# Kernel tuning notes

Hardware: AMD Instinct MI355X
Metric: run time of the kernel (lower is better)

The kernel has to match this reference:

```python
import jax, jax.numpy as jnp
import numpy as np

B, S, D, H = 4, 1024, 1024, 16
DH = D // H  # 64
SCALE = 1.0 / np.sqrt(DH)


def setup_inputs() -> dict:
    key = jax.random.key(0)
    ks = jax.random.split(key, 12)
    std = 0.02
    inp = {
        "query": jax.random.normal(ks[0], (B, S, D), jnp.float32),
        "key": jax.random.normal(ks[1], (B, S, D), jnp.float32),
        "value": jax.random.normal(ks[2], (B, S, D), jnp.float32),
        # all-ones mask: exercises masked_fill path without the NaN the
        # head-axis softmax would produce for any masked entry
        "mask": jnp.ones((1, S, S), jnp.int32),
        "Wq": jax.random.normal(ks[3], (D, D), jnp.float32) * std,
        "bq": jnp.zeros((D,), jnp.float32),
        "Wk": jax.random.normal(ks[4], (D, D), jnp.float32) * std,
        "bk": jnp.zeros((D,), jnp.float32),
        "Wv": jax.random.normal(ks[5], (D, D), jnp.float32) * std,
        "bv": jnp.zeros((D,), jnp.float32),
        "Wo": jax.random.normal(ks[6], (D, D), jnp.float32) * std,
        "bo": jnp.zeros((D,), jnp.float32),
    }
    return inp


def reference(query, key, value, mask, Wq, bq, Wk, bk, Wv, bv, Wo, bo):
    # project and split heads: [B, S, D] -> [B, S, H, DH]
    q = (query @ Wq + bq).reshape(B, S, H, DH)
    k = (key @ Wk + bk).reshape(B, S, H, DH)
    v = (value @ Wv + bv).reshape(B, S, H, DH)

    # scores [B, i, j, H]
    scores = jnp.einsum("bihd,bjhd->bijh", q, k) * SCALE
    # mask [1, i, j] broadcast over heads via trailing axis (unsqueeze(-1))
    scores = jnp.where(mask[..., None] == 0, -jnp.inf, scores)
    # faithful to source: nn.Softmax(dim=-1) on bijh layout -> softmax over HEADS
    attn = jax.nn.softmax(scores, axis=-1)
    # dropout in eval mode (identity)
    x = jnp.einsum("bijh,bjhd->bihd", attn, v).reshape(B, S, D)
    return x @ Wo + bo
```

## Files before the change

### kernel.cpp

```cpp
#include <hip/hip_runtime.h>
#include <hip/hip_bf16.h>


using f32x4  = __attribute__((ext_vector_type(4))) float;
using f32x2  = __attribute__((ext_vector_type(2))) float;
using bf16x8 = __attribute__((ext_vector_type(8))) short;
using bf16x4 = __attribute__((ext_vector_type(4))) short;

__device__ inline unsigned short f2b(float f){
    unsigned u = __float_as_uint(f);
    unsigned r = (u + 0x7fffu + ((u >> 16) & 1u)) >> 16;
    return (unsigned short)r;
}
__device__ inline float b2f(unsigned short s){
    return __uint_as_float(((unsigned)s) << 16);
}

#define GLL16(gp, lp) __builtin_amdgcn_global_load_lds( \
    (const __attribute__((address_space(1))) void*)(gp), \
    (__attribute__((address_space(3))) void*)(lp), 16, 0, 0)

#define LGKM0 do { asm volatile("s_waitcnt lgkmcnt(0)" ::: "memory"); \
                   __builtin_amdgcn_sched_barrier(0); } while(0)
#define BAR   do { __builtin_amdgcn_s_barrier(); \
                   __builtin_amdgcn_sched_barrier(0); } while(0)

__global__ __launch_bounds__(256) void convert_qkv(
    const float* __restrict__ q, const float* __restrict__ k, const float* __restrict__ v,
    unsigned short* __restrict__ dst)
{
    const long gid = (long)blockIdx.x * 256 + threadIdx.x;
    const int  t   = (int)(gid >> 20);
    const long off = (gid & 1048575) << 2;
    const float* src = (t == 0) ? q : (t == 1) ? k : v;
    const float4 x = *(const float4*)(src + off);
    ushort4 o;
    o.x = f2b(x.x); o.y = f2b(x.y); o.z = f2b(x.z); o.w = f2b(x.w);
    *(ushort4*)(dst + (long)t * 4194304 + off) = o;
}

__global__ __launch_bounds__(256) void wtrans(
    const float* __restrict__ w0, const float* __restrict__ w1,
    const float* __restrict__ w2, const float* __restrict__ w3,
    unsigned short* __restrict__ out)
{
    const float* W = (blockIdx.z == 0) ? w0 : (blockIdx.z == 1) ? w1 : (blockIdx.z == 2) ? w2 : w3;
    unsigned short* O = out + (long)blockIdx.z * 1048576;
    __shared__ float t[32][33];
    const int n0 = blockIdx.x * 32, k0 = blockIdx.y * 32;
    const int tx = threadIdx.x, ty = threadIdx.y;
    #pragma unroll
    for (int i = 0; i < 4; i++)
        t[ty + 8*i][tx] = W[(long)(k0 + ty + 8*i) * 1024 + n0 + tx];
    __syncthreads();
    #pragma unroll
    for (int i = 0; i < 4; i++)
        O[(long)(n0 + ty + 8*i) * 1024 + k0 + tx] = f2b(t[tx][ty + 8*i]);
}

__global__ __launch_bounds__(256) void vtrans(
    const unsigned short* __restrict__ V, unsigned short* __restrict__ Vt)
{
    const int b = blockIdx.z;
    __shared__ unsigned short t[32][33];
    const int s0 = blockIdx.x * 32, d0 = blockIdx.y * 32;
    const int tx = threadIdx.x, ty = threadIdx.y;
    #pragma unroll
    for (int i = 0; i < 4; i++)
        t[ty + 8*i][tx] = V[(long)(b*1024 + s0 + ty + 8*i) * 1024 + d0 + tx];
    __syncthreads();
    #pragma unroll
    for (int i = 0; i < 4; i++)
        Vt[(long)b * 1048576 + (long)(d0 + ty + 8*i) * 1024 + s0 + tx] = t[tx][ty + 8*i];
}

template<int OUTF32>
__device__ __forceinline__ void gemm_body(
    const unsigned short* __restrict__ A,
    const unsigned short* __restrict__ BT,
    const float* __restrict__ bias,
    void* __restrict__ Cout, int N, int K,
    unsigned short* As, unsigned short* Bs)
{
    const int tid  = threadIdx.x;
    const int wave = tid >> 6, lane = tid & 63;
    const int l15  = lane & 15, l4 = lane >> 4;
    const int wr   = wave >> 1, wc = wave & 1;
    const long rowBase = (long)blockIdx.x * 128;
    const long colBase = (long)blockIdx.y * 128;

    f32x4 acc[4][4];
    #pragma unroll
    for (int m = 0; m < 4; m++)
        #pragma unroll
        for (int n = 0; n < 4; n++)
            acc[m][n] = (f32x4){0.f, 0.f, 0.f, 0.f};

    const int c0    = wave * 2;
    const int srow0 = c0 * 16 + (lane >> 2);
    const int srow1 = srow0 + 16;
    const int skk   = (lane & 3) * 8;

    for (int k0 = 0; k0 < K; k0 += 32) {
        GLL16(A  + (rowBase + srow0) * K + k0 + skk, As + c0 * 512);
        GLL16(A  + (rowBase + srow1) * K + k0 + skk, As + (c0 + 1) * 512);
        GLL16(BT + (colBase + srow0) * K + k0 + skk, Bs + c0 * 512);
        GLL16(BT + (colBase + srow1) * K + k0 + skk, Bs + (c0 + 1) * 512);
        __syncthreads();
        bf16x8 af[4], bfr[4];
        #pragma unroll
        for (int m = 0; m < 4; m++)
            af[m] = *(const bf16x8*)(As + (wr*64 + m*16 + l15) * 32 + l4 * 8);
        #pragma unroll
        for (int n = 0; n < 4; n++)
            bfr[n] = *(const bf16x8*)(Bs + (wc*64 + n*16 + l15) * 32 + l4 * 8);
        #pragma unroll
        for (int m = 0; m < 4; m++)
            #pragma unroll
            for (int n = 0; n < 4; n++)
                acc[m][n] = __builtin_amdgcn_mfma_f32_16x16x32_bf16(af[m], bfr[n], acc[m][n], 0, 0, 0);
        __syncthreads();
    }

    #pragma unroll
    for (int m = 0; m < 4; m++) {
        const long row = rowBase + wr*64 + m*16 + l4*4;
        #pragma unroll
        for (int n = 0; n < 4; n++) {
            const long col = colBase + wc*64 + n*16 + l15;
            const float bv = bias[col];
            #pragma unroll
            for (int r = 0; r < 4; r++) {
                const float vv = acc[m][n][r] + bv;
                if (OUTF32) ((float*)Cout)[(row + r) * N + col] = vv;
                else        ((unsigned short*)Cout)[(row + r) * N + col] = f2b(vv);
            }
        }
    }
}

__global__ __launch_bounds__(256) void gemm_bias_f32(
    const unsigned short* __restrict__ A,
    const unsigned short* __restrict__ BT,
    const float* __restrict__ bias,
    float* __restrict__ Cout, int N, int K)
{
    __shared__ unsigned short As[128 * 32];
    __shared__ unsigned short Bs[128 * 32];
    gemm_body<1>(A, BT, bias, (void*)Cout, N, K, As, Bs);
}

__global__ __launch_bounds__(256) void gemm3(
    const unsigned short* __restrict__ Abase,
    const unsigned short* __restrict__ WT,
    const float* __restrict__ bq, const float* __restrict__ bk, const float* __restrict__ bv,
    unsigned short* __restrict__ Cbase)
{
    __shared__ unsigned short As[128 * 32];
    __shared__ unsigned short Bs[128 * 32];
    const int z = blockIdx.z;
    const unsigned short* A  = Abase + (long)z * 4194304;
    const unsigned short* BT = WT    + (long)z * 1048576;
    unsigned short*       C  = Cbase + (long)z * 4194304;
    const float* bias = (z == 0) ? bq : (z == 1) ? bk : bv;
    gemm_body<0>(A, BT, bias, (void*)C, 1024, 1024, As, Bs);
}

__global__ __launch_bounds__(512, 2) void attn_fused(
    const unsigned short* __restrict__ Q,
    const unsigned short* __restrict__ Kg_,
    const unsigned short* __restrict__ Vt,
    const int* __restrict__ mask,
    unsigned short* __restrict__ P0,
    unsigned short* __restrict__ P1)
{
    __shared__ __align__(16) unsigned char smem[73728];
    float*         Se = (float*)smem;
    float*         So = (float*)(smem + 36864);
    unsigned char* Pb = smem;

    const int tid = threadIdx.x, w = tid >> 6, lane = tid & 63;
    const int l15 = lane & 15, l4 = lane >> 4;
    const int h0  = 2 * w;
    const int sxor = h0 ^ (l4 << 2);

    const int bid = blockIdx.x;
    const int wg  = (bid & 7) * 32 + (bid >> 3);
    const int b   = wg >> 6;
    const int jh  = (wg >> 5) & 1;
    const int i0  = (wg & 31) << 5;
    const int jbase = jh << 9;

    const unsigned short* Kb = Kg_ + (long)b * 1048576;
    const unsigned short* Vb = Vt  + (long)b * 1048576;
    unsigned short* Pout = (jh == 0) ? P0 : P1;

    const int si = tid >> 4, sj = tid & 15;
    const int xorv = si & 12;
    const int mrow = (i0 + si) * 1024 + jbase;

    bf16x8 qf[2][2][2];
    #pragma unroll
    for (int is = 0; is < 2; is++)
        #pragma unroll
        for (int hh = 0; hh < 2; hh++)
            #pragma unroll
            for (int ks = 0; ks < 2; ks++)
                qf[is][hh][ks] = *(const bf16x8*)(Q + (long)(b*1024 + i0 + is*16 + l15) * 1024
                                                  + (h0 + hh) * 64 + ks * 32 + l4 * 8);

#define LOAD_KF(J0) do { \
    _Pragma("unroll") \
    for (int t_ = 0; t_ < 2; t_++) \
        _Pragma("unroll") \
        for (int hh = 0; hh < 2; hh++) \
            _Pragma("unroll") \
            for (int ks = 0; ks < 2; ks++) \
                kf[t_][hh][ks] = *(const bf16x8*)(Kb + (long)((J0) + t_*16 + l15) * 1024 \
                                                   + (h0 + hh) * 64 + ks * 32 + l4 * 8); \
    } while(0)

#define LOAD_VF(J0) do { \
    _Pragma("unroll") \
    for (int hh = 0; hh < 2; hh++) \
        _Pragma("unroll") \
        for (int n = 0; n < 4; n++) \
            vf[hh][n] = *(const bf16x8*)(Vb + (long)((h0 + hh) * 64 + n * 16 + l15) * 1024 \
                                           + (J0) + l4 * 8); \
    } while(0)

    bf16x8 kf[2][2][2];
    bf16x8 vf[2][4];
    LOAD_KF(jbase);
    LOAD_VF(jbase);

    f32x4 acc[2][2][4];
    #pragma unroll
    for (int is = 0; is < 2; is++)
        #pragma unroll
        for (int hh = 0; hh < 2; hh++)
            #pragma unroll
            for (int n = 0; n < 4; n++)
                acc[is][hh][n] = (f32x4){0.f, 0.f, 0.f, 0.f};

    for (int g = 0; g < 16; ++g) {
        const int j0 = jbase + g * 32;
        const int mke = mask[mrow + g * 32 + sj];
        const int mko = mask[mrow + g * 32 + 16 + sj];

        #pragma unroll
        for (int t_ = 0; t_ < 2; t_++) {
            float* St = t_ ? So : Se;
            #pragma unroll
            for (int is = 0; is < 2; is++) {
                f32x4 sv0 = (f32x4){0.f,0.f,0.f,0.f}, sv1 = (f32x4){0.f,0.f,0.f,0.f};
                sv0 = __builtin_amdgcn_mfma_f32_16x16x32_bf16(qf[is][0][0], kf[t_][0][0], sv0, 0, 0, 0);
                sv0 = __builtin_amdgcn_mfma_f32_16x16x32_bf16(qf[is][0][1], kf[t_][0][1], sv0, 0, 0, 0);
                sv1 = __builtin_amdgcn_mfma_f32_16x16x32_bf16(qf[is][1][0], kf[t_][1][0], sv1, 0, 0, 0);
                sv1 = __builtin_amdgcn_mfma_f32_16x16x32_bf16(qf[is][1][1], kf[t_][1][1], sv1, 0, 0, 0);
                #pragma unroll
                for (int r = 0; r < 4; r++) {
                    const int ij = (is*16 + l4*4 + r) * 16 + l15;
                    f32x2 pr; pr[0] = sv0[r]; pr[1] = sv1[r];
                    *(f32x2*)(St + ij * 18 + sxor) = pr;
                }
            }
        }
        LGKM0; BAR;

        if (g < 15) LOAD_KF(j0 + 32);

        unsigned pe[8];
        {
            const float* sp = Se + tid * 18;
            float tv[16];
            #pragma unroll
            for (int q_ = 0; q_ < 8; q_++) {
                const f32x2 t2 = *(const f32x2*)(sp + q_ * 2);
                tv[q_*2] = t2[0]; tv[q_*2+1] = t2[1];
            }
            float Z = 0.f;
            #pragma unroll
            for (int h = 0; h < 16; h++) {
                float x = tv[h] * 0.18033688f;
                if (mke == 0) x = -__builtin_inff();
                float e; asm("v_exp_f32 %0, %1" : "=v"(e) : "v"(x));
                tv[h] = e; Z += e;
            }
            float inv; asm("v_rcp_f32 %0, %1" : "=v"(inv) : "v"(Z));
            #pragma unroll
            for (int h = 0; h < 8; h++) {
                const unsigned lo = (__float_as_uint(tv[2*h]   * inv) + 0x8000u) >> 16;
                const unsigned hi = (__float_as_uint(tv[2*h+1] * inv) + 0x8000u) >> 16;
                pe[h] = lo | (hi << 16);
            }
        }
        BAR;
        #pragma unroll
        for (int h = 0; h < 16; h++) {
            const unsigned short pv = (unsigned short)((h & 1) ? (pe[h >> 1] >> 16) : pe[h >> 1]);
            *(unsigned short*)(Pb + (h ^ xorv) * 2304 + si * 72 + sj * 2) = pv;
        }

        {
            const float* sp = So + tid * 18;
            float tv[16];
            #pragma unroll
            for (int q_ = 0; q_ < 8; q_++) {
                const f32x2 t2 = *(const f32x2*)(sp + q_ * 2);
                tv[q_*2] = t2[0]; tv[q_*2+1] = t2[1];
            }
            float Z = 0.f;
            #pragma unroll
            for (int h = 0; h < 16; h++) {
                float x = tv[h] * 0.18033688f;
                if (mko == 0) x = -__builtin_inff();
                float e; asm("v_exp_f32 %0, %1" : "=v"(e) : "v"(x));
                tv[h] = e; Z += e;
            }
            float inv; asm("v_rcp_f32 %0, %1" : "=v"(inv) : "v"(Z));
            #pragma unroll
            for (int h = 0; h < 16; h++) {
                const unsigned p16 = (__float_as_uint(tv[h] * inv) + 0x8000u) >> 16;
                *(unsigned short*)(Pb + (h ^ xorv) * 2304 + si * 72 + 32 + sj * 2) = (unsigned short)p16;
            }
        }
        LGKM0; BAR;

        {
            bf16x8 pa[2][2];
            #pragma unroll
            for (int is = 0; is < 2; is++)
                #pragma unroll
                for (int hh = 0; hh < 2; hh++) {
                    const unsigned char* pr = Pb + (h0 + hh) * 2304 + (is*16 + l15) * 72 + l4 * 16;
                    bf16x4 lo = *(const bf16x4*)(pr);
                    bf16x4 hi = *(const bf16x4*)(pr + 8);
                    pa[is][hh] = (bf16x8){lo[0],lo[1],lo[2],lo[3], hi[0],hi[1],hi[2],hi[3]};
                }
            #pragma unroll
            for (int is = 0; is < 2; is++)
                #pragma unroll
                for (int hh = 0; hh < 2; hh++)
                    #pragma unroll
                    for (int n = 0; n < 4; n++)
                        acc[is][hh][n] = __builtin_amdgcn_mfma_f32_16x16x32_bf16(pa[is][hh], vf[hh][n], acc[is][hh][n], 0, 0, 0);
        }
        if (g < 15) {
            LOAD_VF(j0 + 32);
            BAR;
        }
    }

    #pragma unroll
    for (int is = 0; is < 2; is++)
        #pragma unroll
        for (int hh = 0; hh < 2; hh++)
            #pragma unroll
            for (int n = 0; n < 4; n++)
                #pragma unroll
                for (int r = 0; r < 4; r++) {
                    const long row = b * 1024 + i0 + is * 16 + l4 * 4 + r;
                    Pout[row * 1024 + (h0 + hh) * 64 + n * 16 + l15] = f2b(acc[is][hh][n][r]);
                }
#undef LOAD_KF
#undef LOAD_VF
}

__global__ __launch_bounds__(256) void addp(
    unsigned short* __restrict__ P0, const unsigned short* __restrict__ P1)
{
    const long i = ((long)blockIdx.x * 256 + threadIdx.x) * 8;
    ushort4 a0 = *(const ushort4*)(P0 + i);
    ushort4 a1 = *(const ushort4*)(P0 + i + 4);
    ushort4 b0 = *(const ushort4*)(P1 + i);
    ushort4 b1 = *(const ushort4*)(P1 + i + 4);
    ushort4 o0, o1;
    o0.x = f2b(b2f(a0.x) + b2f(b0.x)); o0.y = f2b(b2f(a0.y) + b2f(b0.y));
    o0.z = f2b(b2f(a0.z) + b2f(b0.z)); o0.w = f2b(b2f(a0.w) + b2f(b0.w));
    o1.x = f2b(b2f(a1.x) + b2f(b1.x)); o1.y = f2b(b2f(a1.y) + b2f(b1.y));
    o1.z = f2b(b2f(a1.z) + b2f(b1.z)); o1.w = f2b(b2f(a1.w) + b2f(b1.w));
    *(ushort4*)(P0 + i) = o0;
    *(ushort4*)(P0 + i + 4) = o1;
}

extern "C" void kernel_launch(void* const* d_in, const int* in_sizes, int n_in,
                              void* d_out, int out_size, void* d_ws, size_t ws_size,
                              hipStream_t stream)
{
    const float* q    = (const float*)d_in[0];
    const float* k    = (const float*)d_in[1];
    const float* v    = (const float*)d_in[2];
    const int*   mask = (const int*)  d_in[3];
    const float* Wq   = (const float*)d_in[4];
    const float* bq   = (const float*)d_in[5];
    const float* Wk   = (const float*)d_in[6];
    const float* bk   = (const float*)d_in[7];
    const float* Wv   = (const float*)d_in[8];
    const float* bv   = (const float*)d_in[9];
    const float* Wo   = (const float*)d_in[10];
    const float* bo   = (const float*)d_in[11];

    unsigned short* ws = (unsigned short*)d_ws;
    const long MS = 1048576;
    unsigned short* WT  = ws;
    unsigned short* Xq  = ws + 4*MS;
    unsigned short* Xk  = ws + 8*MS;
    unsigned short* Xv  = ws + 12*MS;
    unsigned short* Qm  = ws + 16*MS;
    unsigned short* Km  = ws + 20*MS;
    unsigned short* Vm  = ws + 24*MS;
    unsigned short* Vtm = Xq;
    unsigned short* P0  = Xk;
    unsigned short* P1  = Vm;

    convert_qkv<<<12288, 256, 0, stream>>>(q, k, v, Xq);
    wtrans<<<dim3(32, 32, 4), dim3(32, 8), 0, stream>>>(Wq, Wk, Wv, Wo, WT);
    gemm3<<<dim3(32, 8, 3), 256, 0, stream>>>(Xq, WT, bq, bk, bv, Qm);
    vtrans<<<dim3(32, 32, 4), dim3(32, 8), 0, stream>>>(Vm, Vtm);
    attn_fused<<<256, 512, 0, stream>>>(Qm, Km, Vtm, mask, P0, P1);
    addp<<<2048, 256, 0, stream>>>(P0, P1);
    gemm_bias_f32<<<dim3(32, 8), 256, 0, stream>>>(P0, WT + 3*MS, bo, (float*)d_out, 1024, 1024);
}
```

Measured before the change: 170.4 us.

## Halve attention query tile to 16 rows and double grid to 512 blocks

```diff
diff --git a/kernel.cpp b/kernel.cpp
--- a/kernel.cpp
+++ b/kernel.cpp
@@ -174,9 +174,8 @@
     unsigned short* __restrict__ P0,
     unsigned short* __restrict__ P1)
 {
-    __shared__ __align__(16) unsigned char smem[73728];
-    float*         Se = (float*)smem;
-    float*         So = (float*)(smem + 36864);
+    __shared__ __align__(16) unsigned char smem[36864];
+    float*         S  = (float*)smem;
     unsigned char* Pb = smem;
 
     const int tid = threadIdx.x, w = tid >> 6, lane = tid & 63;
@@ -185,29 +184,27 @@
     const int sxor = h0 ^ (l4 << 2);
 
     const int bid = blockIdx.x;
-    const int wg  = (bid & 7) * 32 + (bid >> 3);
-    const int b   = wg >> 6;
-    const int jh  = (wg >> 5) & 1;
-    const int i0  = (wg & 31) << 5;
+    const int wg  = (bid & 7) * 64 + (bid >> 3);
+    const int b   = wg >> 7;
+    const int jh  = (wg >> 6) & 1;
+    const int i0  = (wg & 63) << 4;
     const int jbase = jh << 9;
 
     const unsigned short* Kb = Kg_ + (long)b * 1048576;
     const unsigned short* Vb = Vt  + (long)b * 1048576;
     unsigned short* Pout = (jh == 0) ? P0 : P1;
 
-    const int si = tid >> 4, sj = tid & 15;
-    const int xorv = si & 12;
-    const int mrow = (i0 + si) * 1024 + jbase;
-
-    bf16x8 qf[2][2][2];
-    #pragma unroll
-    for (int is = 0; is < 2; is++)
-        #pragma unroll
-        for (int hh = 0; hh < 2; hh++)
-            #pragma unroll
-            for (int ks = 0; ks < 2; ks++)
-                qf[is][hh][ks] = *(const bf16x8*)(Q + (long)(b*1024 + i0 + is*16 + l15) * 1024
-                                                  + (h0 + hh) * 64 + ks * 32 + l4 * 8);
+    const int i_sm = tid >> 5, j_sm = tid & 31;
+    const int xorv = i_sm & 12;
+    const int mrow = (i0 + i_sm) * 1024 + jbase;
+
+    bf16x8 qf[2][2];
+    #pragma unroll
+    for (int hh = 0; hh < 2; hh++)
+        #pragma unroll
+        for (int ks = 0; ks < 2; ks++)
+            qf[hh][ks] = *(const bf16x8*)(Q + (long)(b*1024 + i0 + l15) * 1024
+                                          + (h0 + hh) * 64 + ks * 32 + l4 * 8);
 
 #define LOAD_KF(J0) do { \
     _Pragma("unroll") \
@@ -234,36 +231,29 @@
     LOAD_KF(jbase);
     LOAD_VF(jbase);
 
-    f32x4 acc[2][2][4];
-    #pragma unroll
-    for (int is = 0; is < 2; is++)
-        #pragma unroll
-        for (int hh = 0; hh < 2; hh++)
-            #pragma unroll
-            for (int n = 0; n < 4; n++)
-                acc[is][hh][n] = (f32x4){0.f, 0.f, 0.f, 0.f};
+    f32x4 acc[2][4];
+    #pragma unroll
+    for (int hh = 0; hh < 2; hh++)
+        #pragma unroll
+        for (int n = 0; n < 4; n++)
+            acc[hh][n] = (f32x4){0.f, 0.f, 0.f, 0.f};
 
     for (int g = 0; g < 16; ++g) {
         const int j0 = jbase + g * 32;
-        const int mke = mask[mrow + g * 32 + sj];
-        const int mko = mask[mrow + g * 32 + 16 + sj];
+        const int mk = mask[mrow + g * 32 + j_sm];
 
         #pragma unroll
         for (int t_ = 0; t_ < 2; t_++) {
-            float* St = t_ ? So : Se;
-            #pragma unroll
-            for (int is = 0; is < 2; is++) {
-                f32x4 sv0 = (f32x4){0.f,0.f,0.f,0.f}, sv1 = (f32x4){0.f,0.f,0.f,0.f};
-                sv0 = __builtin_amdgcn_mfma_f32_16x16x32_bf16(qf[is][0][0], kf[t_][0][0], sv0, 0, 0, 0);
-                sv0 = __builtin_amdgcn_mfma_f32_16x16x32_bf16(qf[is][0][1], kf[t_][0][1], sv0, 0, 0, 0);
-                sv1 = __builtin_amdgcn_mfma_f32_16x16x32_bf16(qf[is][1][0], kf[t_][1][0], sv1, 0, 0, 0);
-                sv1 = __builtin_amdgcn_mfma_f32_16x16x32_bf16(qf[is][1][1], kf[t_][1][1], sv1, 0, 0, 0);
-                #pragma unroll
-                for (int r = 0; r < 4; r++) {
-                    const int ij = (is*16 + l4*4 + r) * 16 + l15;
-                    f32x2 pr; pr[0] = sv0[r]; pr[1] = sv1[r];
-                    *(f32x2*)(St + ij * 18 + sxor) = pr;
-                }
+            f32x4 sv0 = (f32x4){0.f,0.f,0.f,0.f}, sv1 = (f32x4){0.f,0.f,0.f,0.f};
+            sv0 = __builtin_amdgcn_mfma_f32_16x16x32_bf16(qf[0][0], kf[t_][0][0], sv0, 0, 0, 0);
+            sv0 = __builtin_amdgcn_mfma_f32_16x16x32_bf16(qf[0][1], kf[t_][0][1], sv0, 0, 0, 0);
+            sv1 = __builtin_amdgcn_mfma_f32_16x16x32_bf16(qf[1][0], kf[t_][1][0], sv1, 0, 0, 0);
+            sv1 = __builtin_amdgcn_mfma_f32_16x16x32_bf16(qf[1][1], kf[t_][1][1], sv1, 0, 0, 0);
+            #pragma unroll
+            for (int r = 0; r < 4; r++) {
+                const int ij = (l4*4 + r) * 32 + t_ * 16 + l15;
+                f32x2 pr; pr[0] = sv0[r]; pr[1] = sv1[r];
+                *(f32x2*)(S + ij * 18 + sxor) = pr;
             }
         }
         LGKM0; BAR;
@@ -272,7 +262,7 @@
 
         unsigned pe[8];
         {
-            const float* sp = Se + tid * 18;
+            const float* sp = S + tid * 18;
             float tv[16];
             #pragma unroll
             for (int q_ = 0; q_ < 8; q_++) {
@@ -283,7 +273,7 @@
             #pragma unroll
             for (int h = 0; h < 16; h++) {
                 float x = tv[h] * 0.18033688f;
-                if (mke == 0) x = -__builtin_inff();
+                if (mk == 0) x = -__builtin_inff();
                 float e; asm("v_exp_f32 %0, %1" : "=v"(e) : "v"(x));
                 tv[h] = e; Z += e;
             }
@@ -299,52 +289,24 @@
         #pragma unroll
         for (int h = 0; h < 16; h++) {
             const unsigned short pv = (unsigned short)((h & 1) ? (pe[h >> 1] >> 16) : pe[h >> 1]);
-            *(unsigned short*)(Pb + (h ^ xorv) * 2304 + si * 72 + sj * 2) = pv;
-        }
+            *(unsigned short*)(Pb + (h ^ xorv) * 1152 + i_sm * 72 + j_sm * 2) = pv;
+        }
+        LGKM0; BAR;
 
         {
-            const float* sp = So + tid * 18;
-            float tv[16];
-            #pragma unroll
-            for (int q_ = 0; q_ < 8; q_++) {
-                const f32x2 t2 = *(const f32x2*)(sp + q_ * 2);
-                tv[q_*2] = t2[0]; tv[q_*2+1] = t2[1];
-            }
-            float Z = 0.f;
-            #pragma unroll
-            for (int h = 0; h < 16; h++) {
-                float x = tv[h] * 0.18033688f;
-                if (mko == 0) x = -__builtin_inff();
-                float e; asm("v_exp_f32 %0, %1" : "=v"(e) : "v"(x));
-                tv[h] = e; Z += e;
-            }
-            float inv; asm("v_rcp_f32 %0, %1" : "=v"(inv) : "v"(Z));
-            #pragma unroll
-            for (int h = 0; h < 16; h++) {
-                const unsigned p16 = (__float_as_uint(tv[h] * inv) + 0x8000u) >> 16;
-                *(unsigned short*)(Pb + (h ^ xorv) * 2304 + si * 72 + 32 + sj * 2) = (unsigned short)p16;
-            }
-        }
-        LGKM0; BAR;
-
-        {
-            bf16x8 pa[2][2];
-            #pragma unroll
-            for (int is = 0; is < 2; is++)
+            bf16x8 pa[2];
+            #pragma unroll
+            for (int hh = 0; hh < 2; hh++) {
+                const unsigned char* pr = Pb + (h0 + hh) * 1152 + l15 * 72 + l4 * 16;
+                bf16x4 lo = *(const bf16x4*)(pr);
+                bf16x4 hi = *(const bf16x4*)(pr + 8);
+                pa[hh] = (bf16x8){lo[0],lo[1],lo[2],lo[3], hi[0],hi[1],hi[2],hi[3]};
+            }
+            #pragma unroll
+            for (int hh = 0; hh < 2; hh++)
                 #pragma unroll
-                for (int hh = 0; hh < 2; hh++) {
-                    const unsigned char* pr = Pb + (h0 + hh) * 2304 + (is*16 + l15) * 72 + l4 * 16;
-                    bf16x4 lo = *(const bf16x4*)(pr);
-                    bf16x4 hi = *(const bf16x4*)(pr + 8);
-                    pa[is][hh] = (bf16x8){lo[0],lo[1],lo[2],lo[3], hi[0],hi[1],hi[2],hi[3]};
-                }
-            #pragma unroll
-            for (int is = 0; is < 2; is++)
-                #pragma unroll
-                for (int hh = 0; hh < 2; hh++)
-                    #pragma unroll
-                    for (int n = 0; n < 4; n++)
-                        acc[is][hh][n] = __builtin_amdgcn_mfma_f32_16x16x32_bf16(pa[is][hh], vf[hh][n], acc[is][hh][n], 0, 0, 0);
+                for (int n = 0; n < 4; n++)
+                    acc[hh][n] = __builtin_amdgcn_mfma_f32_16x16x32_bf16(pa[hh], vf[hh][n], acc[hh][n], 0, 0, 0);
         }
         if (g < 15) {
             LOAD_VF(j0 + 32);
@@ -353,16 +315,14 @@
     }
 
     #pragma unroll
-    for (int is = 0; is < 2; is++)
-        #pragma unroll
-        for (int hh = 0; hh < 2; hh++)
-            #pragma unroll
-            for (int n = 0; n < 4; n++)
-                #pragma unroll
-                for (int r = 0; r < 4; r++) {
-                    const long row = b * 1024 + i0 + is * 16 + l4 * 4 + r;
-                    Pout[row * 1024 + (h0 + hh) * 64 + n * 16 + l15] = f2b(acc[is][hh][n][r]);
-                }
+    for (int hh = 0; hh < 2; hh++)
+        #pragma unroll
+        for (int n = 0; n < 4; n++)
+            #pragma unroll
+            for (int r = 0; r < 4; r++) {
+                const long row = b * 1024 + i0 + l4 * 4 + r;
+                Pout[row * 1024 + (h0 + hh) * 64 + n * 16 + l15] = f2b(acc[hh][n][r]);
+            }
 #undef LOAD_KF
 #undef LOAD_VF
 }
@@ -418,7 +378,7 @@
     wtrans<<<dim3(32, 32, 4), dim3(32, 8), 0, stream>>>(Wq, Wk, Wv, Wo, WT);
     gemm3<<<dim3(32, 8, 3), 256, 0, stream>>>(Xq, WT, bq, bk, bv, Qm);
     vtrans<<<dim3(32, 32, 4), dim3(32, 8), 0, stream>>>(Vm, Vtm);
-    attn_fused<<<256, 512, 0, stream>>>(Qm, Km, Vtm, mask, P0, P1);
+    attn_fused<<<512, 512, 0, stream>>>(Qm, Km, Vtm, mask, P0, P1);
     addp<<<2048, 256, 0, stream>>>(P0, P1);
     gemm_bias_f32<<<dim3(32, 8), 256, 0, stream>>>(P0, WT + 3*MS, bo, (float*)d_out, 1024, 1024);
 }
```

Measured after the change: 223.4 us (median of 2 runs). +31.1%, slower.

## Pre-pack K and V into MFMA fragment order for coalesced attention loads

Applied to the files above, without the earlier changes.

```diff
diff --git a/kernel.cpp b/kernel.cpp
--- a/kernel.cpp
+++ b/kernel.cpp
@@ -58,20 +58,54 @@
         O[(long)(n0 + ty + 8*i) * 1024 + k0 + tx] = f2b(t[tx][ty + 8*i]);
 }
 
-__global__ __launch_bounds__(256) void vtrans(
-    const unsigned short* __restrict__ V, unsigned short* __restrict__ Vt)
-{
-    const int b = blockIdx.z;
-    __shared__ unsigned short t[32][33];
-    const int s0 = blockIdx.x * 32, d0 = blockIdx.y * 32;
-    const int tx = threadIdx.x, ty = threadIdx.y;
-    #pragma unroll
-    for (int i = 0; i < 4; i++)
-        t[ty + 8*i][tx] = V[(long)(b*1024 + s0 + ty + 8*i) * 1024 + d0 + tx];
+__global__ __launch_bounds__(256) void kf_trans(
+    const unsigned short* __restrict__ Km, unsigned short* __restrict__ Kf)
+{
+    const int b = blockIdx.y, jt = blockIdx.x;
+    __shared__ unsigned short t[16][1032];
+    const int tid = threadIdx.x;
+    #pragma unroll
+    for (int p = 0; p < 8; p++) {
+        const int idx = p * 2048 + tid * 8;
+        const int r = idx >> 10, c = idx & 1023;
+        *(uint4*)&t[r][c] = *(const uint4*)(Km + (long)(b*1024 + jt*16 + r) * 1024 + c);
+    }
     __syncthreads();
     #pragma unroll
-    for (int i = 0; i < 4; i++)
-        Vt[(long)b * 1048576 + (long)(d0 + ty + 8*i) * 1024 + s0 + tx] = t[tx][ty + 8*i];
+    for (int p = 0; p < 8; p++) {
+        const int o  = p * 2048 + tid * 8;
+        const int hk = o >> 9;
+        const int l  = (o >> 3) & 63;
+        const int cc = (hk >> 1) * 64 + (hk & 1) * 32 + (l >> 4) * 8;
+        *(uint4*)(Kf + (long)(b*64 + jt) * 16384 + o) = *(const uint4*)&t[l & 15][cc];
+    }
+}
+
+__global__ __launch_bounds__(256) void vf_trans(
+    const unsigned short* __restrict__ Vm, unsigned short* __restrict__ Vf)
+{
+    const int b = blockIdx.y, jg = blockIdx.x;
+    __shared__ unsigned short t[32][1032];
+    const int tid = threadIdx.x;
+    #pragma unroll
+    for (int p = 0; p < 16; p++) {
+        const int idx = p * 2048 + tid * 8;
+        const int r = idx >> 10, c = idx & 1023;
+        *(uint4*)&t[r][c] = *(const uint4*)(Vm + (long)(b*1024 + jg*32 + r) * 1024 + c);
+    }
+    __syncthreads();
+    #pragma unroll
+    for (int p = 0; p < 16; p++) {
+        const int o  = p * 2048 + tid * 8;
+        const int hn = o >> 9;
+        const int l  = (o >> 3) & 63;
+        const int col = (hn >> 2) * 64 + (hn & 3) * 16 + (l & 15);
+        const int r0  = (l >> 4) * 8;
+        unsigned short vv[8];
+        #pragma unroll
+        for (int e = 0; e < 8; e++) vv[e] = t[r0 + e][col];
+        *(uint4*)(Vf + (long)(b*32 + jg) * 32768 + o) = *(const uint4*)vv;
+    }
 }
 
 template<int OUTF32>
@@ -168,8 +202,8 @@
 
 __global__ __launch_bounds__(512, 2) void attn_fused(
     const unsigned short* __restrict__ Q,
-    const unsigned short* __restrict__ Kg_,
-    const unsigned short* __restrict__ Vt,
+    const unsigned short* __restrict__ Kf_,
+    const unsigned short* __restrict__ Vf_,
     const int* __restrict__ mask,
     unsigned short* __restrict__ P0,
     unsigned short* __restrict__ P1)
@@ -191,8 +225,8 @@
     const int i0  = (wg & 31) << 5;
     const int jbase = jh << 9;
 
-    const unsigned short* Kb = Kg_ + (long)b * 1048576;
-    const unsigned short* Vb = Vt  + (long)b * 1048576;
+    const unsigned short* Kfb = Kf_ + (long)b * 1048576;
+    const unsigned short* Vfb = Vf_ + (long)b * 1048576;
     unsigned short* Pout = (jh == 0) ? P0 : P1;
 
     const int si = tid >> 4, sj = tid & 15;
@@ -209,30 +243,30 @@
                 qf[is][hh][ks] = *(const bf16x8*)(Q + (long)(b*1024 + i0 + is*16 + l15) * 1024
                                                   + (h0 + hh) * 64 + ks * 32 + l4 * 8);
 
-#define LOAD_KF(J0) do { \
+#define LOAD_KF(JT) do { \
     _Pragma("unroll") \
     for (int t_ = 0; t_ < 2; t_++) \
         _Pragma("unroll") \
         for (int hh = 0; hh < 2; hh++) \
             _Pragma("unroll") \
             for (int ks = 0; ks < 2; ks++) \
-                kf[t_][hh][ks] = *(const bf16x8*)(Kb + (long)((J0) + t_*16 + l15) * 1024 \
-                                                   + (h0 + hh) * 64 + ks * 32 + l4 * 8); \
+                kf[t_][hh][ks] = *(const bf16x8*)(Kfb + ((JT) + t_) * 16384 \
+                                                   + ((h0 + hh) * 2 + ks) * 512 + lane * 8); \
     } while(0)
 
-#define LOAD_VF(J0) do { \
+#define LOAD_VF(JG) do { \
     _Pragma("unroll") \
     for (int hh = 0; hh < 2; hh++) \
         _Pragma("unroll") \
         for (int n = 0; n < 4; n++) \
-            vf[hh][n] = *(const bf16x8*)(Vb + (long)((h0 + hh) * 64 + n * 16 + l15) * 1024 \
-                                           + (J0) + l4 * 8); \
+            vf[hh][n] = *(const bf16x8*)(Vfb + (long)(JG) * 32768 \
+                                           + ((h0 + hh) * 4 + n) * 512 + lane * 8); \
     } while(0)
 
     bf16x8 kf[2][2][2];
     bf16x8 vf[2][4];
-    LOAD_KF(jbase);
-    LOAD_VF(jbase);
+    LOAD_KF(jh*32);
+    LOAD_VF(jh*16);
 
     f32x4 acc[2][2][4];
     #pragma unroll
@@ -244,7 +278,6 @@
                 acc[is][hh][n] = (f32x4){0.f, 0.f, 0.f, 0.f};
 
     for (int g = 0; g < 16; ++g) {
-        const int j0 = jbase + g * 32;
         const int mke = mask[mrow + g * 32 + sj];
         const int mko = mask[mrow + g * 32 + 16 + sj];
 
@@ -268,7 +301,7 @@
         }
         LGKM0; BAR;
 
-        if (g < 15) LOAD_KF(j0 + 32);
+        if (g < 15) LOAD_KF(jh*32 + (g + 1) * 2);
 
         unsigned pe[8];
         {
@@ -347,7 +380,7 @@
                         acc[is][hh][n] = __builtin_amdgcn_mfma_f32_16x16x32_bf16(pa[is][hh], vf[hh][n], acc[is][hh][n], 0, 0, 0);
         }
         if (g < 15) {
-            LOAD_VF(j0 + 32);
+            LOAD_VF(jh*16 + g + 1);
             BAR;
         }
     }
@@ -410,15 +443,17 @@
     unsigned short* Qm  = ws + 16*MS;
     unsigned short* Km  = ws + 20*MS;
     unsigned short* Vm  = ws + 24*MS;
-    unsigned short* Vtm = Xq;
+    unsigned short* Kf  = Xq;
+    unsigned short* Vf  = Xv;
     unsigned short* P0  = Xk;
     unsigned short* P1  = Vm;
 
     convert_qkv<<<12288, 256, 0, stream>>>(q, k, v, Xq);
     wtrans<<<dim3(32, 32, 4), dim3(32, 8), 0, stream>>>(Wq, Wk, Wv, Wo, WT);
     gemm3<<<dim3(32, 8, 3), 256, 0, stream>>>(Xq, WT, bq, bk, bv, Qm);
-    vtrans<<<dim3(32, 32, 4), dim3(32, 8), 0, stream>>>(Vm, Vtm);
-    attn_fused<<<256, 512, 0, stream>>>(Qm, Km, Vtm, mask, P0, P1);
+    kf_trans<<<dim3(64, 4), 256, 0, stream>>>(Km, Kf);
+    vf_trans<<<dim3(32, 4), 256, 0, stream>>>(Vm, Vf);
+    attn_fused<<<256, 512, 0, stream>>>(Qm, Kf, Vf, mask, P0, P1);
     addp<<<2048, 256, 0, stream>>>(P0, P1);
     gemm_bias_f32<<<dim3(32, 8), 256, 0, stream>>>(P0, WT + 3*MS, bo, (float*)d_out, 1024, 1024);
 }
```

New measurement: 157.4 us. -7.6%, faster.
